# Optimization experiments

Hardware: AMD Instinct MI355X
Metric: run time of the kernel (lower is better)

Reference implementation:

```python
import jax, jax.numpy as jnp
import numpy as np

IN_CH = 1024   # backbone channels
N_T = 81       # n_targets (COCO classes + bg)
K = 7          # PSROI grid size
H = 100        # feature map height
WID = 100      # feature map width
R = 1024       # number of regions
S = 2          # bilinear sampling points per bin edge (PSROIAlign-style average)


def setup_inputs() -> dict:
    key = jax.random.key(0)
    k1, k2, k3 = jax.random.split(key, 3)
    x = jax.random.normal(k1, (IN_CH, H, WID), dtype=jnp.float32)
    # regions: fractional (i, j, h, w) = (center_y, center_x, height, width) in [0,1]
    regions = jax.random.uniform(k2, (R, 4), dtype=jnp.float32)
    conv_w = jax.random.normal(k3, (N_T * K * K, IN_CH), dtype=jnp.float32) * 0.02
    conv_b = jnp.zeros((N_T * K * K,), dtype=jnp.float32)
    return {"x": x, "regions": regions, "conv_w": conv_w, "conv_b": conv_b}


def _bilinear_pool(map_thw, ys, xs):
    """Average of bilinear samples of one bin's score map.

    map_thw: (T, H, W) score map for this (u, v) bin's channel group.
    ys: (R, S) sample row coords.  xs: (R, S) sample col coords.
    Returns (R, T): per-region average-pooled bin value.
    """
    Hm, Wm = map_thw.shape[1], map_thw.shape[2]
    ys = jnp.clip(ys, 0.0, Hm - 1)
    xs = jnp.clip(xs, 0.0, Wm - 1)
    y0 = jnp.floor(ys)
    x0 = jnp.floor(xs)
    y0i = y0.astype(jnp.int32)
    x0i = x0.astype(jnp.int32)
    y1i = jnp.minimum(y0i + 1, Hm - 1)
    x1i = jnp.minimum(x0i + 1, Wm - 1)
    wy1 = ys - y0
    wy0 = 1.0 - wy1
    wx1 = xs - x0
    wx0 = 1.0 - wx1

    def g(yi, xi):  # gather (T, R, S, S)
        return map_thw[:, yi[:, :, None], xi[:, None, :]]

    v = (g(y0i, x0i) * (wy0[:, :, None] * wx0[:, None, :])
         + g(y0i, x1i) * (wy0[:, :, None] * wx1[:, None, :])
         + g(y1i, x0i) * (wy1[:, :, None] * wx0[:, None, :])
         + g(y1i, x1i) * (wy1[:, :, None] * wx1[:, None, :]))
    return v.mean((2, 3)).T  # (R, T)


def reference(x, regions, conv_w, conv_b):
    # 1x1 conv score map: (n_targets*k^2, H, W)
    sm = jnp.einsum('oc,chw->ohw', conv_w, x) + conv_b[:, None, None]
    sm = sm.reshape(N_T, K, K, H, WID)  # (T, ky, kx, H, W) position-sensitive groups

    # region geometry (fractional center/size -> absolute feature-map coords)
    top = (regions[:, 0] - regions[:, 2] * 0.5) * H     # (R,)
    left = (regions[:, 1] - regions[:, 3] * 0.5) * WID  # (R,)
    bh = regions[:, 2] * H / K                          # bin height
    bw = regions[:, 3] * WID / K                        # bin width

    off = (jnp.arange(S, dtype=jnp.float32) + 0.5) / S  # (S,) sample offsets in bin
    bins = jnp.arange(K, dtype=jnp.float32)             # (K,)
    ys = top[:, None, None] + (bins[None, :, None] + off[None, None, :]) * bh[:, None, None]   # (R,K,S)
    xs = left[:, None, None] + (bins[None, :, None] + off[None, None, :]) * bw[:, None, None]  # (R,K,S)

    # vmap over the k x k position-sensitive bins; bin (u,v) reads channel group (:,u,v)
    inner = jax.vmap(_bilinear_pool, in_axes=(1, None, 1))  # over kx: sm axis, xs axis
    outer = jax.vmap(inner, in_axes=(1, 1, None))           # over ky: sm axis, ys axis
    pooled = outer(sm, ys, xs)  # (K, K, R, T)

    # pooled.mean(-1).mean(-1) over the k x k grid
    scores = pooled.mean((0, 1))  # (R, T)
    return scores
```

## Files before the change

### kernel.cpp

```cpp
#include <hip/hip_runtime.h>
#include <cstddef>

#define IN_CH 1024
#define NT    81
#define KGRID 7
#define NBINS 49
#define HH    100
#define WW    100
#define NPIX  (HH*WW)
#define NREG  1024
#define COLB  82
#define NCOL  (NBINS*COLB)
#define NPADW 4096
#define SROW  NCOL
#define NG    8
#define PXB   ((NPIX + 31) / 32)
#define PXG   (PXB * (IN_CH / 128))
#define PREPG (PXG + NPADW)

typedef unsigned short ushortT;
typedef short bf16x8 __attribute__((ext_vector_type(8)));
typedef float f32x4  __attribute__((ext_vector_type(4)));

static __device__ __forceinline__ unsigned short f2bf(float f) {
    unsigned int u = __builtin_bit_cast(unsigned int, f);
    return (unsigned short)((u + 0x7fffu + ((u >> 16) & 1u)) >> 16);
}
static __device__ __forceinline__ float bf_lo(unsigned int v) {
    return __builtin_bit_cast(float, v << 16);
}
static __device__ __forceinline__ float bf_hi(unsigned int v) {
    return __builtin_bit_cast(float, v & 0xffff0000u);
}

static __device__ __forceinline__ void gld_lds16(const ushortT* g, ushortT* l) {
    __builtin_amdgcn_global_load_lds(
        (__attribute__((address_space(1))) void*)(unsigned long long)(uintptr_t)g,
        (__attribute__((address_space(3))) void*)(unsigned int)(unsigned long long)(uintptr_t)l,
        16, 0, 0);
}

__global__ __launch_bounds__(256) void prep_fused(const float* __restrict__ x,
                                                  ushortT* __restrict__ xbT,
                                                  const float* __restrict__ conv_w,
                                                  ushortT* __restrict__ Wr) {
    __shared__ float tile[128][33];
    const int tid = threadIdx.x;
    const int bid = blockIdx.x;
    if (bid < PXG) {
        const int p0 = (bid % PXB) * 32;
        const int c0 = (bid / PXB) * 128;
        const int pl = tid & 31;
        const int cg = tid >> 5;
        const int p = p0 + pl;
#pragma unroll
        for (int it = 0; it < 16; ++it) {
            const int c = it * 8 + cg;
            tile[c][pl] = (p < NPIX) ? x[(size_t)(c0 + c) * NPIX + p] : 0.0f;
        }
        __syncthreads();
#pragma unroll
        for (int pass = 0; pass < 2; ++pass) {
            const int pix = pass * 16 + (tid >> 4);
            const int cb  = (tid & 15) * 8;
            if (p0 + pix < NPIX) {
                uint4 pk;
                pk.x = (unsigned int)f2bf(tile[cb + 0][pix]) | ((unsigned int)f2bf(tile[cb + 1][pix]) << 16);
                pk.y = (unsigned int)f2bf(tile[cb + 2][pix]) | ((unsigned int)f2bf(tile[cb + 3][pix]) << 16);
                pk.z = (unsigned int)f2bf(tile[cb + 4][pix]) | ((unsigned int)f2bf(tile[cb + 5][pix]) << 16);
                pk.w = (unsigned int)f2bf(tile[cb + 6][pix]) | ((unsigned int)f2bf(tile[cb + 7][pix]) << 16);
                *(uint4*)(xbT + (size_t)(p0 + pix) * IN_CH + c0 + cb) = pk;
            }
        }
    } else {
        const int row = bid - PXG;
        const int bin = row / COLB;
        const int t   = row - bin * COLB;
        const int c   = tid * 4;
        uint2 pk; pk.x = 0; pk.y = 0;
        if (bin < NBINS && t < NT) {
            const float4 v = *(const float4*)(conv_w + ((size_t)(t * NBINS + bin)) * IN_CH + c);
            pk.x = (unsigned int)f2bf(v.x) | ((unsigned int)f2bf(v.y) << 16);
            pk.y = (unsigned int)f2bf(v.z) | ((unsigned int)f2bf(v.w) << 16);
        }
        *(uint2*)(Wr + (size_t)row * IN_CH + c) = pk;
    }
}

__global__ __launch_bounds__(256) void gemm_sm(const ushortT* __restrict__ xbT,
                                               const ushortT* __restrict__ Wr,
                                               ushortT* __restrict__ sm) {
    __shared__ ushortT a_lds[128 * 32];
    __shared__ ushortT b_lds[128 * 32];
    const int tid  = threadIdx.x;
    const int lane = tid & 63;
    const int w    = tid >> 6;
    const int wm   = w & 1;
    const int wn   = w >> 1;
    const int n0   = blockIdx.x * 128;
    const int p0   = blockIdx.y * 128;

    const int srow0 = w * 32 + (lane >> 2);
    const int scol  = (lane & 3) * 8;
    int ap0 = p0 + srow0;      if (ap0 > NPIX - 1) ap0 = NPIX - 1;
    int ap1 = p0 + srow0 + 16; if (ap1 > NPIX - 1) ap1 = NPIX - 1;
    const ushortT* ag0 = xbT + (size_t)ap0 * IN_CH + scol;
    const ushortT* ag1 = xbT + (size_t)ap1 * IN_CH + scol;
    const ushortT* bg0 = Wr + (size_t)(n0 + srow0) * IN_CH + scol;
    const ushortT* bg1 = Wr + (size_t)(n0 + srow0 + 16) * IN_CH + scol;
    ushortT* al0 = a_lds + (w * 32) * 32;
    ushortT* al1 = a_lds + (w * 32 + 16) * 32;
    ushortT* bl0 = b_lds + (w * 32) * 32;
    ushortT* bl1 = b_lds + (w * 32 + 16) * 32;

    const int m_lane = lane & 15;
    const int k0     = (lane >> 4) * 8;

    f32x4 acc[4][4];
#pragma unroll
    for (int mt = 0; mt < 4; ++mt)
#pragma unroll
        for (int nt = 0; nt < 4; ++nt) acc[mt][nt] = (f32x4){0.f, 0.f, 0.f, 0.f};

    for (int kc = 0; kc < IN_CH / 32; ++kc) {
        __syncthreads();
        gld_lds16(ag0, al0);
        gld_lds16(ag1, al1);
        gld_lds16(bg0, bl0);
        gld_lds16(bg1, bl1);
        ag0 += 32; ag1 += 32; bg0 += 32; bg1 += 32;
        __syncthreads();

        bf16x8 af[4], bf[4];
#pragma unroll
        for (int mt = 0; mt < 4; ++mt)
            af[mt] = *(const bf16x8*)(a_lds + (wm * 64 + mt * 16 + m_lane) * 32 + k0);
#pragma unroll
        for (int nt = 0; nt < 4; ++nt)
            bf[nt] = *(const bf16x8*)(b_lds + (wn * 64 + nt * 16 + m_lane) * 32 + k0);
#pragma unroll
        for (int mt = 0; mt < 4; ++mt)
#pragma unroll
            for (int nt = 0; nt < 4; ++nt)
                acc[mt][nt] = __builtin_amdgcn_mfma_f32_16x16x32_bf16(af[mt], bf[nt], acc[mt][nt], 0, 0, 0);
    }

    const int prow_base = p0 + wm * 64 + (lane >> 4) * 4;
    const int ncol_base = n0 + wn * 64 + m_lane;
#pragma unroll
    for (int mt = 0; mt < 4; ++mt) {
#pragma unroll
        for (int rg = 0; rg < 4; ++rg) {
            const int p = prow_base + mt * 16 + rg;
            if (p < NPIX) {
                ushortT* rowp = sm + (size_t)p * SROW;
#pragma unroll
                for (int nt = 0; nt < 4; ++nt) {
                    const int n = ncol_base + nt * 16;
                    if (n < NCOL) rowp[n] = f2bf(acc[mt][nt][rg]);
                }
            }
        }
    }
}

__global__ __launch_bounds__(256) void pool_kernel(const ushortT* __restrict__ sm,
                                                   const float* __restrict__ regions,
                                                   const float* __restrict__ conv_b,
                                                   float* __restrict__ out) {
    __shared__ int   rowo[28]; __shared__ float roww[28];
    __shared__ int   coli[28]; __shared__ float colw[28];
    __shared__ int   pofs[108];
    __shared__ float pw[108];
    __shared__ float part[12][84];
    const int tid = threadIdx.x;
    const int r = blockIdx.x;
    const int g = blockIdx.y;

    if (tid < 28) {
        const float4 reg = *(const float4*)(regions + (size_t)r * 4);
        const float top = (reg.x - reg.z * 0.5f) * (float)HH;
        const float bh  = reg.z * ((float)HH / (float)KGRID);
        const int u = tid >> 2, i = tid & 3;
        const int s = i >> 1, hi = i & 1;
        float y = top + ((float)u + ((float)s + 0.5f) * 0.5f) * bh;
        y = fminf(fmaxf(y, 0.0f), (float)(HH - 1));
        const float y0f = floorf(y);
        const int y0 = (int)y0f;
        const float wy1 = y - y0f;
        rowo[tid] = (hi ? min(y0 + 1, HH - 1) : y0) * WW;
        roww[tid] = hi ? wy1 : (1.0f - wy1);
    } else if (tid >= 32 && tid < 60) {
        const float4 reg = *(const float4*)(regions + (size_t)r * 4);
        const float left = (reg.y - reg.w * 0.5f) * (float)WW;
        const float bw   = reg.w * ((float)WW / (float)KGRID);
        const int idx = tid - 32;
        const int v = idx >> 2, j = idx & 3;
        const int s = j >> 1, hi = j & 1;
        float xx = left + ((float)v + ((float)s + 0.5f) * 0.5f) * bw;
        xx = fminf(fmaxf(xx, 0.0f), (float)(WW - 1));
        const float x0f = floorf(xx);
        const int x0 = (int)x0f;
        const float wx1 = xx - x0f;
        coli[idx] = hi ? min(x0 + 1, WW - 1) : x0;
        colw[idx] = hi ? wx1 : (1.0f - wx1);
    }
    __syncthreads();
    if (tid < 108) {
        if (tid < 98) {
            const int tt = g * 98 + tid;
            const int bin = tt >> 4, tap = tt & 15;
            const int u = bin / KGRID, v = bin - u * KGRID;
            const int i = tap >> 2, j = tap & 3;
            const int pix = rowo[u * 4 + i] + coli[v * 4 + j];
            pofs[tid] = pix * SROW + bin * COLB;
            pw[tid]   = roww[u * 4 + i] * colw[v * 4 + j] * (1.0f / 196.0f);
        } else {
            pofs[tid] = 0;
            pw[tid]   = 0.0f;
        }
    }
    __syncthreads();

    const int lane = tid & 63, w = tid >> 6;
    const int sub  = lane / 21;
    const int cidx = lane - sub * 21;
    if (sub < 3) {
        const int str = w * 3 + sub;
        const int l2  = cidx * 4;
        uint2 v[9];
#pragma unroll
        for (int it = 0; it < 9; ++it)
            v[it] = *(const uint2*)(sm + pofs[str * 9 + it] + l2);
        float a0 = 0.f, a1 = 0.f, a2 = 0.f, a3 = 0.f;
#pragma unroll
        for (int it = 0; it < 9; ++it) {
            const float wt = pw[str * 9 + it];
            a0 += wt * bf_lo(v[it].x); a1 += wt * bf_hi(v[it].x);
            a2 += wt * bf_lo(v[it].y); a3 += wt * bf_hi(v[it].y);
        }
        float4 p4; p4.x = a0; p4.y = a1; p4.z = a2; p4.w = a3;
        *(float4*)&part[str][l2] = p4;
    }
    __syncthreads();
    if (tid < NT) {
        float v = 0.f;
#pragma unroll
        for (int s = 0; s < 12; ++s) v += part[s][tid];
        if (g == 0) {
            float bsum = 0.f;
            for (int bin = 0; bin < NBINS; ++bin) bsum += conv_b[tid * NBINS + bin];
            v += bsum * (1.0f / (float)NBINS);
        }
        atomicAdd(out + (size_t)r * NT + tid, v);
    }
}

__global__ __launch_bounds__(256) void xpose_kernel(const float* __restrict__ x,
                                                    float* __restrict__ xt) {
    __shared__ float tile[32][33];
    const int p0 = blockIdx.x * 32;
    const int c0 = blockIdx.y * 32;
    const int tx = threadIdx.x;
    const int ty = threadIdx.y;
#pragma unroll
    for (int k = 0; k < 32; k += 8) {
        const int p = p0 + tx;
        if (p < NPIX) tile[ty + k][tx] = x[(size_t)(c0 + ty + k) * NPIX + p];
    }
    __syncthreads();
#pragma unroll
    for (int k = 0; k < 32; k += 8) {
        const int p = p0 + ty + k;
        if (p < NPIX) xt[(size_t)p * IN_CH + (c0 + tx)] = tile[tx][ty + k];
    }
}

template <bool XPOSED>
__global__ __launch_bounds__(256) void psroi_kernel(
    const float* __restrict__ xsrc, const float* __restrict__ regions,
    const float* __restrict__ conv_w, const float* __restrict__ conv_b,
    float* __restrict__ out) {
    __shared__ float w_lds[32 * 96];
    __shared__ float g_lds[32 * 64];
    __shared__ int   rowoff[64][4];
    __shared__ float rowwf[64][4];
    __shared__ int   colidx[64][4];
    __shared__ float colwf[64][4];
    const int tid = threadIdx.x;
    const int bin = blockIdx.x >> 4;
    const int rg  = blockIdx.x & 15;
    const int u = bin / KGRID, v = bin % KGRID;
    const int r0 = rg * 64;
    if (tid < 64) {
        const float4 reg = *(const float4*)(regions + (size_t)(r0 + tid) * 4);
        const float top  = (reg.x - reg.z * 0.5f) * (float)HH;
        const float left = (reg.y - reg.w * 0.5f) * (float)WW;
        const float bh = reg.z * ((float)HH / (float)KGRID);
        const float bw = reg.w * ((float)WW / (float)KGRID);
        const float scale = 1.0f / 196.0f;
#pragma unroll
        for (int s = 0; s < 2; s++) {
            const float off = (s + 0.5f) * 0.5f;
            float yy = top + ((float)u + off) * bh;
            yy = fminf(fmaxf(yy, 0.0f), (float)(HH - 1));
            const float y0f = floorf(yy);
            const int y0 = (int)y0f;
            const float wy1 = yy - y0f;
            rowoff[tid][2 * s] = y0 * WW;
            rowoff[tid][2 * s + 1] = min(y0 + 1, HH - 1) * WW;
            rowwf[tid][2 * s] = (1.0f - wy1) * scale;
            rowwf[tid][2 * s + 1] = wy1 * scale;
            float xx = left + ((float)v + off) * bw;
            xx = fminf(fmaxf(xx, 0.0f), (float)(WW - 1));
            const float x0f = floorf(xx);
            const int x0 = (int)x0f;
            const float wx1 = xx - x0f;
            colidx[tid][2 * s] = x0;
            colidx[tid][2 * s + 1] = min(x0 + 1, WW - 1);
            colwf[tid][2 * s] = 1.0f - wx1;
            colwf[tid][2 * s + 1] = wx1;
        }
    }
    const int ri = tid & 15, tq = tid >> 4, rb = tid >> 2, cq = tid & 3;
    float acc[4][6];
#pragma unroll
    for (int m = 0; m < 4; m++)
#pragma unroll
        for (int k = 0; k < 6; k++) acc[m][k] = 0.0f;
    for (int chunk = 0; chunk < IN_CH / 32; chunk++) {
        const int c0 = chunk * 32;
        __syncthreads();
#pragma unroll
        for (int it = 0; it < 12; it++) {
            const int idx = it * 256 + tid;
            const int t = idx >> 5, c = idx & 31;
            float val = 0.0f;
            if (t < NT) val = conv_w[(size_t)(t * NBINS + bin) * IN_CH + c0 + c];
            w_lds[c * 96 + t] = val;
        }
        const int cbase = c0 + cq * 8;
        float g8[8];
#pragma unroll
        for (int cc = 0; cc < 8; cc++) g8[cc] = 0.0f;
#pragma unroll
        for (int i = 0; i < 4; i++) {
            const int ro = rowoff[rb][i];
            const float wy = rowwf[rb][i];
#pragma unroll
            for (int j = 0; j < 4; j++) {
                const int pix = ro + colidx[rb][j];
                const float wv = wy * colwf[rb][j];
                if (XPOSED) {
                    const float4* p = (const float4*)(xsrc + (size_t)pix * IN_CH + cbase);
                    const float4 a = p[0]; const float4 b = p[1];
                    g8[0] += wv * a.x; g8[1] += wv * a.y; g8[2] += wv * a.z; g8[3] += wv * a.w;
                    g8[4] += wv * b.x; g8[5] += wv * b.y; g8[6] += wv * b.z; g8[7] += wv * b.w;
                } else {
#pragma unroll
                    for (int cc = 0; cc < 8; cc++)
                        g8[cc] += wv * xsrc[(size_t)(cbase + cc) * NPIX + pix];
                }
            }
        }
#pragma unroll
        for (int cc = 0; cc < 8; cc++) g_lds[(cq * 8 + cc) * 64 + rb] = g8[cc];
        __syncthreads();
#pragma unroll 4
        for (int c = 0; c < 32; c++) {
            float wv[6];
#pragma unroll
            for (int k = 0; k < 6; k++) wv[k] = w_lds[c * 96 + tq * 6 + k];
            const float4 gq = *(const float4*)&g_lds[c * 64 + ri * 4];
            const float gm[4] = {gq.x, gq.y, gq.z, gq.w};
#pragma unroll
            for (int m = 0; m < 4; m++)
#pragma unroll
                for (int k = 0; k < 6; k++) acc[m][k] += gm[m] * wv[k];
        }
    }
    const float invK2 = 1.0f / 49.0f;
#pragma unroll
    for (int k = 0; k < 6; k++) {
        const int t = tq * 6 + k;
        if (t < NT) {
            const float bterm = conv_b[t * NBINS + bin] * invK2;
#pragma unroll
            for (int m = 0; m < 4; m++) {
                const int rr = r0 + ri * 4 + m;
                atomicAdd(&out[(size_t)rr * NT + t], acc[m][k] + bterm);
            }
        }
    }
}

extern "C" void kernel_launch(void* const* d_in, const int* in_sizes, int n_in,
                              void* d_out, int out_size, void* d_ws, size_t ws_size,
                              hipStream_t stream) {
    const float* x       = (const float*)d_in[0];
    const float* regions = (const float*)d_in[1];
    const float* conv_w  = (const float*)d_in[2];
    const float* conv_b  = (const float*)d_in[3];
    float* out = (float*)d_out;

    const size_t sz_xbT = (size_t)NPIX * IN_CH * 2;
    const size_t sz_Wr  = (size_t)NPADW * IN_CH * 2;
    const size_t sz_sm  = (size_t)NPIX * SROW * 2 + 256;
    const size_t need   = sz_xbT + sz_Wr + sz_sm;

    if (ws_size >= need) {
        ushortT* xbT = (ushortT*)d_ws;
        ushortT* Wr  = (ushortT*)((char*)d_ws + sz_xbT);
        ushortT* sm  = (ushortT*)((char*)d_ws + sz_xbT + sz_Wr);
        hipMemsetAsync(out, 0, (size_t)out_size * sizeof(float), stream);
        prep_fused<<<dim3(PREPG), 256, 0, stream>>>(x, xbT, conv_w, Wr);
        gemm_sm<<<dim3(NPADW / 128, (NPIX + 127) / 128), 256, 0, stream>>>(xbT, Wr, sm);
        pool_kernel<<<dim3(NREG, NG), 256, 0, stream>>>(sm, regions, conv_b, out);
    } else {
        hipMemsetAsync(out, 0, (size_t)out_size * sizeof(float), stream);
        const size_t xt_bytes = (size_t)NPIX * IN_CH * sizeof(float);
        const dim3 mainGrid(NBINS * 16);
        if (ws_size >= xt_bytes) {
            float* xt = (float*)d_ws;
            xpose_kernel<<<dim3((NPIX + 31) / 32, IN_CH / 32), dim3(32, 8), 0, stream>>>(x, xt);
            psroi_kernel<true><<<mainGrid, 256, 0, stream>>>(xt, regions, conv_w, conv_b, out);
        } else {
            psroi_kernel<false><<<mainGrid, 256, 0, stream>>>(x, regions, conv_w, conv_b, out);
        }
    }
}
```

Measured before the change: 233.4 us.

## Quantize score map to int8 with per-tile scales to cut pool traffic

The GEMM epilogue now takes the per-block absolute maximum through an LDS reduction, stores a per-tile scale, and writes the score map as int8 with bins padded to 84 bytes instead of bf16. The pool kernel reads 4 bytes per lane rather than 8 and dequantizes using the tile scales, choosing between the two adjacent column tiles per element. This halves the score-map write and gather bandwidth but adds a block reduction to the GEMM and extra scale loads and selects in pooling. Quantization error grows with the tile max and may be too large for the tolerance.

```diff
diff --git a/kernel.cpp b/kernel.cpp
--- a/kernel.cpp
+++ b/kernel.cpp
@@ -12,8 +12,11 @@
 #define COLB  82
 #define NCOL  (NBINS*COLB)
 #define NPADW 4096
-#define SROW  NCOL
+#define SBIN  84
+#define SROWB (NBINS*SBIN)
 #define NG    8
+#define NPT   79
+#define NSC   2560
 #define PXB   ((NPIX + 31) / 32)
 #define PXG   (PXB * (IN_CH / 128))
 #define PREPG (PXG + NPADW)
@@ -25,12 +28,6 @@
 static __device__ __forceinline__ unsigned short f2bf(float f) {
     unsigned int u = __builtin_bit_cast(unsigned int, f);
     return (unsigned short)((u + 0x7fffu + ((u >> 16) & 1u)) >> 16);
-}
-static __device__ __forceinline__ float bf_lo(unsigned int v) {
-    return __builtin_bit_cast(float, v << 16);
-}
-static __device__ __forceinline__ float bf_hi(unsigned int v) {
-    return __builtin_bit_cast(float, v & 0xffff0000u);
 }
 
 static __device__ __forceinline__ void gld_lds16(const ushortT* g, ushortT* l) {
@@ -89,7 +86,8 @@
 
 __global__ __launch_bounds__(256) void gemm_sm(const ushortT* __restrict__ xbT,
                                                const ushortT* __restrict__ Wr,
-                                               ushortT* __restrict__ sm) {
+                                               unsigned char* __restrict__ sm,
+                                               float* __restrict__ scales) {
     __shared__ ushortT a_lds[128 * 32];
     __shared__ ushortT b_lds[128 * 32];
     const int tid  = threadIdx.x;
@@ -145,26 +143,57 @@
                 acc[mt][nt] = __builtin_amdgcn_mfma_f32_16x16x32_bf16(af[mt], bf[nt], acc[mt][nt], 0, 0, 0);
     }
 
+    float am = 0.0f;
+#pragma unroll
+    for (int mt = 0; mt < 4; ++mt)
+#pragma unroll
+        for (int nt = 0; nt < 4; ++nt)
+#pragma unroll
+            for (int rg = 0; rg < 4; ++rg)
+                am = fmaxf(am, fabsf(acc[mt][nt][rg]));
+    __syncthreads();
+    float* red = (float*)a_lds;
+    red[tid] = am;
+    __syncthreads();
+#pragma unroll
+    for (int s = 128; s > 0; s >>= 1) {
+        if (tid < s) red[tid] = fmaxf(red[tid], red[tid + s]);
+        __syncthreads();
+    }
+    const float amax = fmaxf(red[0], 1e-30f);
+    const float inv  = 127.0f / amax;
+    if (tid == 0) scales[blockIdx.y * 32 + blockIdx.x] = amax * (1.0f / 127.0f);
+
     const int prow_base = p0 + wm * 64 + (lane >> 4) * 4;
     const int ncol_base = n0 + wn * 64 + m_lane;
+    int  coloff[4];
+    bool cok[4];
+#pragma unroll
+    for (int nt = 0; nt < 4; ++nt) {
+        const int n = ncol_base + nt * 16;
+        cok[nt] = (n < NCOL);
+        coloff[nt] = n + 2 * (n / COLB);
+    }
 #pragma unroll
     for (int mt = 0; mt < 4; ++mt) {
 #pragma unroll
         for (int rg = 0; rg < 4; ++rg) {
             const int p = prow_base + mt * 16 + rg;
             if (p < NPIX) {
-                ushortT* rowp = sm + (size_t)p * SROW;
-#pragma unroll
-                for (int nt = 0; nt < 4; ++nt) {
-                    const int n = ncol_base + nt * 16;
-                    if (n < NCOL) rowp[n] = f2bf(acc[mt][nt][rg]);
-                }
+                unsigned char* rowp = sm + (size_t)p * SROWB;
+#pragma unroll
+                for (int nt = 0; nt < 4; ++nt)
+                    if (cok[nt]) {
+                        const int q = __float2int_rn(acc[mt][nt][rg] * inv);
+                        rowp[coloff[nt]] = (unsigned char)(signed char)q;
+                    }
             }
         }
     }
 }
 
-__global__ __launch_bounds__(256) void pool_kernel(const ushortT* __restrict__ sm,
+__global__ __launch_bounds__(256) void pool_kernel(const unsigned char* __restrict__ sm,
+                                                   const float* __restrict__ scales,
                                                    const float* __restrict__ regions,
                                                    const float* __restrict__ conv_b,
                                                    float* __restrict__ out) {
@@ -172,6 +201,8 @@
     __shared__ int   coli[28]; __shared__ float colw[28];
     __shared__ int   pofs[108];
     __shared__ float pw[108];
+    __shared__ int   pptb[108];
+    __shared__ int   pnb[108];
     __shared__ float part[12][84];
     const int tid = threadIdx.x;
     const int r = blockIdx.x;
@@ -213,11 +244,15 @@
             const int u = bin / KGRID, v = bin - u * KGRID;
             const int i = tap >> 2, j = tap & 3;
             const int pix = rowo[u * 4 + i] + coli[v * 4 + j];
-            pofs[tid] = pix * SROW + bin * COLB;
+            pofs[tid] = pix * SROWB + bin * SBIN;
             pw[tid]   = roww[u * 4 + i] * colw[v * 4 + j] * (1.0f / 196.0f);
+            pptb[tid] = (pix >> 7) * 32;
+            pnb[tid]  = bin * COLB;
         } else {
             pofs[tid] = 0;
             pw[tid]   = 0.0f;
+            pptb[tid] = 0;
+            pnb[tid]  = 0;
         }
     }
     __syncthreads();
@@ -227,20 +262,33 @@
     const int cidx = lane - sub * 21;
     if (sub < 3) {
         const int str = w * 3 + sub;
-        const int l2  = cidx * 4;
-        uint2 v[9];
+        const int l4  = cidx * 4;
+        unsigned int v[9];
 #pragma unroll
         for (int it = 0; it < 9; ++it)
-            v[it] = *(const uint2*)(sm + pofs[str * 9 + it] + l2);
+            v[it] = *(const unsigned int*)(sm + pofs[str * 9 + it] + l4);
         float a0 = 0.f, a1 = 0.f, a2 = 0.f, a3 = 0.f;
 #pragma unroll
         for (int it = 0; it < 9; ++it) {
-            const float wt = pw[str * 9 + it];
-            a0 += wt * bf_lo(v[it].x); a1 += wt * bf_hi(v[it].x);
-            a2 += wt * bf_lo(v[it].y); a3 += wt * bf_hi(v[it].y);
+            const int lt = str * 9 + it;
+            const int nb  = pnb[lt] + l4;
+            const int nt0 = nb >> 7;
+            const int rr  = nb & 127;
+            const float s0 = scales[pptb[lt] + nt0];
+            const float s1 = scales[pptb[lt] + nt0 + 1];
+            const float wt = pw[lt];
+            const float w0 = wt * s0, w1 = wt * s1;
+            const int q0 = (int)(signed char)(v[it] & 0xff);
+            const int q1 = (int)(signed char)((v[it] >> 8) & 0xff);
+            const int q2 = (int)(signed char)((v[it] >> 16) & 0xff);
+            const int q3 = (int)(signed char)(v[it] >> 24);
+            a0 += ((rr < 128) ? w0 : w1) * (float)q0;
+            a1 += ((rr < 127) ? w0 : w1) * (float)q1;
+            a2 += ((rr < 126) ? w0 : w1) * (float)q2;
+            a3 += ((rr < 125) ? w0 : w1) * (float)q3;
         }
         float4 p4; p4.x = a0; p4.y = a1; p4.z = a2; p4.w = a3;
-        *(float4*)&part[str][l2] = p4;
+        *(float4*)&part[str][l4] = p4;
     }
     __syncthreads();
     if (tid < NT) {
@@ -405,17 +453,19 @@
 
     const size_t sz_xbT = (size_t)NPIX * IN_CH * 2;
     const size_t sz_Wr  = (size_t)NPADW * IN_CH * 2;
-    const size_t sz_sm  = (size_t)NPIX * SROW * 2 + 256;
-    const size_t need   = sz_xbT + sz_Wr + sz_sm;
+    const size_t sz_sm  = (size_t)NPIX * SROWB + 256;
+    const size_t sz_sc  = (size_t)NSC * sizeof(float);
+    const size_t need   = sz_xbT + sz_Wr + sz_sm + sz_sc;
 
     if (ws_size >= need) {
         ushortT* xbT = (ushortT*)d_ws;
         ushortT* Wr  = (ushortT*)((char*)d_ws + sz_xbT);
-        ushortT* sm  = (ushortT*)((char*)d_ws + sz_xbT + sz_Wr);
+        unsigned char* sm = (unsigned char*)d_ws + sz_xbT + sz_Wr;
+        float* scales = (float*)((char*)d_ws + sz_xbT + sz_Wr + sz_sm);
         hipMemsetAsync(out, 0, (size_t)out_size * sizeof(float), stream);
         prep_fused<<<dim3(PREPG), 256, 0, stream>>>(x, xbT, conv_w, Wr);
-        gemm_sm<<<dim3(NPADW / 128, (NPIX + 127) / 128), 256, 0, stream>>>(xbT, Wr, sm);
-        pool_kernel<<<dim3(NREG, NG), 256, 0, stream>>>(sm, regions, conv_b, out);
+        gemm_sm<<<dim3(NPADW / 128, (NPIX + 127) / 128), 256, 0, stream>>>(xbT, Wr, sm, scales);
+        pool_kernel<<<dim3(NREG, NG), 256, 0, stream>>>(sm, scales, regions, conv_b, out);
     } else {
         hipMemsetAsync(out, 0, (size_t)out_size * sizeof(float), stream);
         const size_t xt_bytes = (size_t)NPIX * IN_CH * sizeof(float);
```

Result: no change. 237.8 us (+1.9%).
